# Kernel optimization log

Hardware: AMD Instinct MI355X
Metric: run time of the kernel (lower is better)

Reference implementation:

```python
import jax, jax.numpy as jnp
import numpy as np

B, L, D_MODEL, H = 2, 2048, 1024, 16
HD = D_MODEL // H  # head dim = 64


def setup_inputs() -> dict:
    key = jax.random.key(0)
    ks = jax.random.split(key, 11)
    s = 1.0 / np.sqrt(D_MODEL)
    inp = {
        "Q": jax.random.normal(ks[0], (B, L, D_MODEL), jnp.float32),
        "K": jax.random.normal(ks[1], (B, L, D_MODEL), jnp.float32),
        "V": jax.random.normal(ks[2], (B, L, D_MODEL), jnp.float32),
        "Wq": jax.random.normal(ks[3], (D_MODEL, D_MODEL), jnp.float32) * s,
        "bq": jnp.zeros((D_MODEL,), jnp.float32),
        "Wk": jax.random.normal(ks[4], (D_MODEL, D_MODEL), jnp.float32) * s,
        "bk": jnp.zeros((D_MODEL,), jnp.float32),
        "Wv": jax.random.normal(ks[5], (D_MODEL, D_MODEL), jnp.float32) * s,
        "bv": jnp.zeros((D_MODEL,), jnp.float32),
        "Wo": jax.random.normal(ks[6], (D_MODEL, D_MODEL), jnp.float32) * s,
        "bo": jnp.zeros((D_MODEL,), jnp.float32),
    }
    return inp


def _split_heads(x):
    # [B, L, H*D] -> [B, H, L, D]
    return x.reshape(B, L, H, HD).transpose(0, 2, 1, 3)


def reference(Q, K, V, Wq, bq, Wk, bk, Wv, bv, Wo, bo):
    q = _split_heads(Q @ Wq.T + bq)
    k = _split_heads(K @ Wk.T + bk)
    v = _split_heads(V @ Wv.T + bv)
    scale = 1.0 / jnp.sqrt(jnp.asarray(HD, q.dtype))
    # full [B, H, L, L] score matrix, as in the original bmm->softmax->bmm
    scores = jnp.einsum("bhqd,bhkd->bhqk", q, k) * scale
    attn = jax.nn.softmax(scores, axis=-1)
    o = jnp.einsum("bhqk,bhkd->bhqd", attn, v)
    o = o.transpose(0, 2, 1, 3).reshape(B, L, D_MODEL)  # concat heads
    return o @ Wo.T + bo
```

## Files before the change

### kernel.cpp

```cpp
#include <hip/hip_runtime.h>
#include <math.h>
#include <stdint.h>

typedef __bf16 bf16_t;
typedef __attribute__((ext_vector_type(2))) __bf16 bf16x2;
typedef __attribute__((ext_vector_type(8))) __bf16 bf16x8;
typedef __attribute__((ext_vector_type(4))) float f32x4;
typedef __attribute__((ext_vector_type(16))) float f32x16;
typedef __attribute__((address_space(1))) unsigned int gu32;
typedef __attribute__((address_space(3))) unsigned int lu32;

#define MFMA16(a, b, c) __builtin_amdgcn_mfma_f32_16x16x32_bf16((a), (b), (c), 0, 0, 0)
#define MFMA32(a, b, c) __builtin_amdgcn_mfma_f32_32x32x16_bf16((a), (b), (c), 0, 0, 0)

__device__ __forceinline__ void gll16(const void* g, void* l) {
    __builtin_amdgcn_global_load_lds((const gu32*)(uintptr_t)g,
                                     (lu32*)(uintptr_t)l, 16, 0, 0);
}

__device__ __forceinline__ bf16x8 ld_frag68(const bf16_t* p) {
    union { bf16x8 v; uint2 u[2]; } r;
    r.u[0] = *(const uint2*)p;
    r.u[1] = *(const uint2*)(p + 4);
    return r.v;
}

__global__ __launch_bounds__(256) void convert_all(
    const float* __restrict__ Q, const float* __restrict__ K, const float* __restrict__ V,
    const float* __restrict__ Wq, const float* __restrict__ Wk, const float* __restrict__ Wv,
    const float* __restrict__ Wo, bf16_t* __restrict__ dst) {
    size_t e0 = (size_t)blockIdx.x * 2048;
    const float* src; size_t off;
    if (e0 < 4194304)       { src = Q;  off = e0; }
    else if (e0 < 8388608)  { src = K;  off = e0 - 4194304; }
    else if (e0 < 12582912) { src = V;  off = e0 - 8388608; }
    else if (e0 < 13631488) { src = Wq; off = e0 - 12582912; }
    else if (e0 < 14680064) { src = Wk; off = e0 - 13631488; }
    else if (e0 < 15728640) { src = Wv; off = e0 - 14680064; }
    else                    { src = Wo; off = e0 - 15728640; }
#pragma unroll
    for (int p = 0; p < 2; ++p) {
        int t = p * 1024 + threadIdx.x * 4;
        float4 v = *(const float4*)(src + off + t);
        union { ushort4 u; bf16_t h[4]; } pk;
        pk.h[0] = (bf16_t)v.x; pk.h[1] = (bf16_t)v.y;
        pk.h[2] = (bf16_t)v.z; pk.h[3] = (bf16_t)v.w;
        *(ushort4*)(dst + e0 + t) = pk.u;
    }
}

__global__ __launch_bounds__(256) void qkv_gemm(
    const bf16_t* __restrict__ Qb, const bf16_t* __restrict__ Kb, const bf16_t* __restrict__ Vb,
    const bf16_t* __restrict__ Wqb, const bf16_t* __restrict__ Wkb, const bf16_t* __restrict__ Wvb,
    const float* __restrict__ bq, const float* __restrict__ bk, const float* __restrict__ bv,
    bf16_t* __restrict__ qo, bf16_t* __restrict__ ko, bf16_t* __restrict__ vT) {
    constexpr int Kdim = 1024, N = 1024;
    __shared__ __attribute__((aligned(16))) bf16_t smem[2 * 128 * 64];
    bf16_t* As = smem;
    bf16_t* Bs = smem + 128 * 64;

    const int tid = threadIdx.x, wave = tid >> 6, lane = tid & 63;
    const int z = blockIdx.z;
    const bf16_t* A = (z == 0) ? Qb : (z == 1) ? Kb : Vb;
    const bf16_t* W = (z == 0) ? Wqb : (z == 1) ? Wkb : Wvb;
    const float* bias = (z == 0) ? bq : (z == 1) ? bk : bv;
    const int bm = blockIdx.x * 128, bn = blockIdx.y * 128;
    const int l16 = lane & 15, quad = lane >> 4;
    const int wm = (wave >> 1) * 64, wn = (wave & 1) * 64;
    const int grow = lane >> 3, gcol = (lane & 7) * 8;

    f32x4 acc[4][4] = {};

    for (int k0 = 0; k0 < Kdim; k0 += 64) {
#pragma unroll
        for (int j = 0; j < 4; ++j) {
            int chunk = wave * 4 + j;
            int row = chunk * 8 + grow;
            gll16(A + (size_t)(bm + row) * Kdim + k0 + gcol, As + chunk * 512);
            gll16(W + (size_t)(bn + row) * Kdim + k0 + gcol, Bs + chunk * 512);
        }
        __syncthreads();
#pragma unroll
        for (int ks = 0; ks < 64; ks += 32) {
            bf16x8 af[4], bf[4];
#pragma unroll
            for (int i = 0; i < 4; ++i)
                af[i] = *(const bf16x8*)&As[(wm + i * 16 + l16) * 64 + ks + quad * 8];
#pragma unroll
            for (int i = 0; i < 4; ++i)
                bf[i] = *(const bf16x8*)&Bs[(wn + i * 16 + l16) * 64 + ks + quad * 8];
#pragma unroll
            for (int i = 0; i < 4; ++i)
#pragma unroll
                for (int j = 0; j < 4; ++j)
                    acc[i][j] = MFMA16(af[i], bf[j], acc[i][j]);
        }
        __syncthreads();
    }

    if (z < 2) {
        bf16_t* outp = (z == 0) ? qo : ko;
        const float sc = (z == 0) ? 0.18033688011112042f : 1.0f;
        constexpr int RST = 132;
#pragma unroll
        for (int p = 0; p < 2; ++p) {
            __syncthreads();
            if ((wave >> 1) == p) {
#pragma unroll
                for (int mi = 0; mi < 4; ++mi)
#pragma unroll
                    for (int nj = 0; nj < 4; ++nj) {
                        int col = wn + nj * 16 + l16;
                        float bv_ = bias[bn + col];
#pragma unroll
                        for (int r = 0; r < 4; ++r) {
                            int rp = mi * 16 + quad * 4 + r;
                            smem[rp * RST + col] = (bf16_t)((acc[mi][nj][r] + bv_) * sc);
                        }
                    }
            }
            __syncthreads();
            int rp = tid >> 2;
            int cb = (tid & 3) * 32;
            int row = bm + p * 64 + rp;
#pragma unroll
            for (int j = 0; j < 4; ++j) {
                uint2 lo = *(const uint2*)&smem[rp * RST + cb + j * 8];
                uint2 hi = *(const uint2*)&smem[rp * RST + cb + j * 8 + 4];
                *(uint4*)&outp[(size_t)row * N + bn + cb + j * 8] =
                    make_uint4(lo.x, lo.y, hi.x, hi.y);
            }
        }
    } else {
#pragma unroll
        for (int mi = 0; mi < 4; ++mi)
#pragma unroll
            for (int nj = 0; nj < 4; ++nj) {
                int col = bn + wn + nj * 16 + l16;
                int h = col >> 6, d = col & 63;
                float bv_ = bias[col];
                int row0 = bm + wm + mi * 16 + quad * 4;
                int bb = row0 >> 11, l = row0 & 2047;
                int lb = (l & ~12) | ((l & 4) << 1) | ((l & 8) >> 1);
                union { ushort4 u; bf16_t h4[4]; } pk;
#pragma unroll
                for (int r = 0; r < 4; ++r) pk.h4[r] = (bf16_t)(acc[mi][nj][r] + bv_);
                *(ushort4*)&vT[(((size_t)bb * 16 + h) * 64 + d) * 2048 + lb] = pk.u;
            }
    }
}

__global__ __launch_bounds__(256) void out_gemm(const bf16_t* __restrict__ A,
                                                const bf16_t* __restrict__ W,
                                                const float* __restrict__ bias,
                                                float* __restrict__ out) {
    constexpr int Kdim = 1024, N = 1024;
    __shared__ __attribute__((aligned(16))) bf16_t As[64 * 64];
    __shared__ __attribute__((aligned(16))) bf16_t Bs[128 * 64];
    const int tid = threadIdx.x, wave = tid >> 6, lane = tid & 63;
    const int bm = blockIdx.x * 64, bn = blockIdx.y * 128;
    const int l16 = lane & 15, quad = lane >> 4;
    const int wm = (wave >> 1) * 32, wn = (wave & 1) * 64;
    const int grow = lane >> 3, gcol = (lane & 7) * 8;
    f32x4 acc[2][4] = {};

    for (int k0 = 0; k0 < Kdim; k0 += 64) {
#pragma unroll
        for (int j = 0; j < 2; ++j) {
            int chunk = wave * 2 + j;
            int row = chunk * 8 + grow;
            gll16(A + (size_t)(bm + row) * Kdim + k0 + gcol, As + chunk * 512);
        }
#pragma unroll
        for (int j = 0; j < 4; ++j) {
            int chunk = wave * 4 + j;
            int row = chunk * 8 + grow;
            gll16(W + (size_t)(bn + row) * Kdim + k0 + gcol, Bs + chunk * 512);
        }
        __syncthreads();
#pragma unroll
        for (int ks = 0; ks < 64; ks += 32) {
            bf16x8 af[2], bf[4];
#pragma unroll
            for (int i = 0; i < 2; ++i)
                af[i] = *(const bf16x8*)&As[(wm + i * 16 + l16) * 64 + ks + quad * 8];
#pragma unroll
            for (int i = 0; i < 4; ++i)
                bf[i] = *(const bf16x8*)&Bs[(wn + i * 16 + l16) * 64 + ks + quad * 8];
#pragma unroll
            for (int i = 0; i < 2; ++i)
#pragma unroll
                for (int j = 0; j < 4; ++j)
                    acc[i][j] = MFMA16(af[i], bf[j], acc[i][j]);
        }
        __syncthreads();
    }
#pragma unroll
    for (int mi = 0; mi < 2; ++mi)
#pragma unroll
        for (int nj = 0; nj < 4; ++nj) {
            int col = bn + wn + nj * 16 + l16;
            float bv_ = bias[col];
#pragma unroll
            for (int r = 0; r < 4; ++r) {
                int row = bm + wm + mi * 16 + quad * 4 + r;
                out[(size_t)row * N + col] = acc[mi][nj][r] + bv_;
            }
        }
}

__global__ __launch_bounds__(256, 4) void attn6(const bf16_t* __restrict__ qo,
                                                const bf16_t* __restrict__ ko,
                                                const bf16_t* __restrict__ vT,
                                                bf16_t* __restrict__ Op,
                                                float* __restrict__ lpp) {
    constexpr int L = 2048, D = 1024, ST = 68;
    __shared__ __attribute__((aligned(16))) bf16_t smem[2 * 64 * ST];
    bf16_t* ksm = smem;
    bf16_t* vsm = smem + 64 * ST;

    const int tid = threadIdx.x, wave = tid >> 6, lane = tid & 63;
    const int l31 = lane & 31, hi = lane >> 5;
    const int b = blockIdx.x >> 4, h = blockIdx.x & 15;
    const int q0 = blockIdx.y * 128;
    const int split = blockIdx.z;
    bf16_t* Opart = Op + (size_t)split * 4194304;
    float* lpart = lpp + split * 65536;

    const int rloc = tid >> 2, cg = tid & 3;
    const bf16_t* kbase = ko + ((size_t)b * L + rloc) * D + h * 64 + cg * 16;
    const bf16_t* vbase = vT + (((size_t)b * 16 + h) * 64 + rloc) * L + cg * 16;

    bf16x8 qf[4];
    {
        const bf16_t* qptr = qo + ((size_t)b * L + q0 + wave * 32 + l31) * D + h * 64 + hi * 8;
#pragma unroll
        for (int ks = 0; ks < 4; ++ks) qf[ks] = *(const bf16x8*)(qptr + ks * 16);
    }

    f32x16 o0{}, o1{};
    float lpl = 0.f;

    const int kt0 = split * 16, kt1 = kt0 + 16;
    for (int kt = kt0; kt < kt1; ++kt) {
        const size_t koff = (size_t)(kt * 64) * D;
        const int voff = kt * 64;
        uint4 ka = *(const uint4*)(kbase + koff);
        uint4 kc = *(const uint4*)(kbase + koff + 8);
        uint4 va = *(const uint4*)(vbase + voff);
        uint4 vc = *(const uint4*)(vbase + voff + 8);
        __syncthreads();
        {
            bf16_t* kd = &ksm[rloc * ST + cg * 16];
            bf16_t* vd = &vsm[rloc * ST + cg * 16];
            *(uint2*)(kd + 0)  = make_uint2(ka.x, ka.y);
            *(uint2*)(kd + 4)  = make_uint2(ka.z, ka.w);
            *(uint2*)(kd + 8)  = make_uint2(kc.x, kc.y);
            *(uint2*)(kd + 12) = make_uint2(kc.z, kc.w);
            *(uint2*)(vd + 0)  = make_uint2(va.x, va.y);
            *(uint2*)(vd + 4)  = make_uint2(va.z, va.w);
            *(uint2*)(vd + 8)  = make_uint2(vc.x, vc.y);
            *(uint2*)(vd + 12) = make_uint2(vc.z, vc.w);
        }
        __syncthreads();

        f32x16 s0{}, s1{};
#pragma unroll
        for (int ks = 0; ks < 4; ++ks) {
            bf16x8 k0 = ld_frag68(&ksm[l31 * ST + ks * 16 + hi * 8]);
            bf16x8 k1 = ld_frag68(&ksm[(32 + l31) * ST + ks * 16 + hi * 8]);
            s0 = MFMA32(k0, qf[ks], s0);
            s1 = MFMA32(k1, qf[ks], s1);
        }

#pragma unroll
        for (int t = 0; t < 4; ++t) {
            union { bf16x8 v; bf16_t e[8]; } pf;
#pragma unroll
            for (int j = 0; j < 8; ++j) {
                float sv = (t < 2) ? s0[(t & 1) * 8 + j] : s1[(t & 1) * 8 + j];
                float p = __builtin_amdgcn_exp2f(sv);
                lpl += p;
                pf.e[j] = (bf16_t)p;
            }
            bf16x8 v0 = ld_frag68(&vsm[l31 * ST + t * 16 + hi * 8]);
            bf16x8 v1 = ld_frag68(&vsm[(32 + l31) * ST + t * 16 + hi * 8]);
            o0 = MFMA32(v0, pf.v, o0);
            o1 = MFMA32(v1, pf.v, o1);
        }
    }

    lpl += __shfl_xor(lpl, 32, 64);
    if (hi == 0)
        lpart[((size_t)b * 16 + h) * 2048 + q0 + wave * 32 + l31] = lpl;

    __syncthreads();
    bf16_t* ew = smem + wave * (32 * ST);
#pragma unroll
    for (int r = 0; r < 16; r += 2) {
        int d = (r & 3) + 8 * (r >> 2) + 4 * hi;
        *(bf16x2*)&ew[l31 * ST + d] = bf16x2{(bf16_t)o0[r], (bf16_t)o0[r + 1]};
        *(bf16x2*)&ew[l31 * ST + 32 + d] = bf16x2{(bf16_t)o1[r], (bf16_t)o1[r + 1]};
    }
#pragma unroll
    for (int p = 0; p < 4; ++p) {
        int rr = p * 8 + (lane >> 3);
        int cc = (lane & 7) * 8;
        uint2 lo = *(const uint2*)&ew[rr * ST + cc];
        uint2 hi2 = *(const uint2*)&ew[rr * ST + cc + 4];
        *(uint4*)&Opart[((size_t)b * L + q0 + wave * 32 + rr) * D + h * 64 + cc] =
            make_uint4(lo.x, lo.y, hi2.x, hi2.y);
    }
}

__global__ __launch_bounds__(256) void combine(const bf16_t* __restrict__ Op,
                                               const float* __restrict__ lpp,
                                               bf16_t* __restrict__ Ob) {
    const size_t c = (size_t)blockIdx.x * 256 + threadIdx.x;
    const int bl = (int)(c >> 7);
    const int h = ((int)c >> 3) & 15;
    const int bb = bl >> 11, l = bl & 2047;
    const int li = (bb * 16 + h) * 2048 + l;
    const float inv = 1.f / (lpp[li] + lpp[65536 + li]);
    union { uint4 u; bf16_t h8[8]; } a, b, o;
    a.u = *(const uint4*)(Op + c * 8);
    b.u = *(const uint4*)(Op + 4194304 + c * 8);
#pragma unroll
    for (int i = 0; i < 8; ++i)
        o.h8[i] = (bf16_t)(((float)a.h8[i] + (float)b.h8[i]) * inv);
    *(uint4*)(Ob + c * 8) = o.u;
}

extern "C" void kernel_launch(void* const* d_in, const int* in_sizes, int n_in,
                              void* d_out, int out_size, void* d_ws, size_t ws_size,
                              hipStream_t stream) {
    const float* Q  = (const float*)d_in[0];
    const float* Kx = (const float*)d_in[1];
    const float* V  = (const float*)d_in[2];
    const float* Wq = (const float*)d_in[3];
    const float* bq = (const float*)d_in[4];
    const float* Wk = (const float*)d_in[5];
    const float* bk = (const float*)d_in[6];
    const float* Wv = (const float*)d_in[7];
    const float* bv = (const float*)d_in[8];
    const float* Wo = (const float*)d_in[9];
    const float* bo = (const float*)d_in[10];

    bf16_t* ws0 = (bf16_t*)d_ws;
    bf16_t* Qb  = ws0;
    bf16_t* Kb  = ws0 + 4194304;
    bf16_t* Vb  = ws0 + 8388608;
    bf16_t* Wqb = ws0 + 12582912;
    bf16_t* Wkb = ws0 + 13631488;
    bf16_t* Wvb = ws0 + 14680064;
    bf16_t* Wob = ws0 + 15728640;
    bf16_t* vT  = ws0 + 16777216;
    bf16_t* Op  = Qb;
    bf16_t* Obf = Vb;
    float*  lpp = (float*)Wqb;
    bf16_t* qo = (bf16_t*)d_out;
    bf16_t* ko = qo + 4194304;

    convert_all<<<8192, 256, 0, stream>>>(Q, Kx, V, Wq, Wk, Wv, Wo, ws0);
    qkv_gemm<<<dim3(32, 8, 3), 256, 0, stream>>>(Qb, Kb, Vb, Wqb, Wkb, Wvb,
                                                 bq, bk, bv, qo, ko, vT);
    attn6<<<dim3(32, 16, 2), 256, 0, stream>>>(qo, ko, vT, Op, lpp);
    combine<<<2048, 256, 0, stream>>>(Op, lpp, Obf);
    out_gemm<<<dim3(64, 8), 256, 0, stream>>>(Obf, Wob, bo, (float*)d_out);
}
```

Measured before the change: 234.3 us.

## Double-buffer LDS tiles in QKV and output projection GEMMs

Both projection GEMMs now hold two LDS buffers. The global_load_lds for the next K tile is issued before the MFMA compute on the current tile, with one vmcnt wait and one barrier per iteration instead of two __syncthreads. This is meant to hide global-memory latency behind the matrix math. The cost is double the LDS footprint (64KB per block in qkv_gemm), which may reduce occupancy.

```diff
diff --git a/kernel.cpp b/kernel.cpp
--- a/kernel.cpp
+++ b/kernel.cpp
@@ -55,9 +55,7 @@
     const float* __restrict__ bq, const float* __restrict__ bk, const float* __restrict__ bv,
     bf16_t* __restrict__ qo, bf16_t* __restrict__ ko, bf16_t* __restrict__ vT) {
     constexpr int Kdim = 1024, N = 1024;
-    __shared__ __attribute__((aligned(16))) bf16_t smem[2 * 128 * 64];
-    bf16_t* As = smem;
-    bf16_t* Bs = smem + 128 * 64;
+    __shared__ __attribute__((aligned(16))) bf16_t smem[4 * 128 * 64];
 
     const int tid = threadIdx.x, wave = tid >> 6, lane = tid & 63;
     const int z = blockIdx.z;
@@ -71,7 +69,7 @@
 
     f32x4 acc[4][4] = {};
 
-    for (int k0 = 0; k0 < Kdim; k0 += 64) {
+    auto stage = [&](int k0, bf16_t* As, bf16_t* Bs) {
 #pragma unroll
         for (int j = 0; j < 4; ++j) {
             int chunk = wave * 4 + j;
@@ -79,7 +77,8 @@
             gll16(A + (size_t)(bm + row) * Kdim + k0 + gcol, As + chunk * 512);
             gll16(W + (size_t)(bn + row) * Kdim + k0 + gcol, Bs + chunk * 512);
         }
-        __syncthreads();
+    };
+    auto compute = [&](const bf16_t* As, const bf16_t* Bs) {
 #pragma unroll
         for (int ks = 0; ks < 64; ks += 32) {
             bf16x8 af[4], bf[4];
@@ -95,7 +94,24 @@
                 for (int j = 0; j < 4; ++j)
                     acc[i][j] = MFMA16(af[i], bf[j], acc[i][j]);
         }
-        __syncthreads();
+    };
+
+    stage(0, smem, smem + 8192);
+    asm volatile("s_waitcnt vmcnt(0)" ::: "memory");
+    __builtin_amdgcn_s_barrier();
+    int cur = 0;
+    for (int t = 0; t < 15; ++t) {
+        bf16_t* nb = smem + (cur ^ 1) * 16384;
+        stage((t + 1) * 64, nb, nb + 8192);
+        bf16_t* cb = smem + cur * 16384;
+        compute(cb, cb + 8192);
+        asm volatile("s_waitcnt vmcnt(0)" ::: "memory");
+        __builtin_amdgcn_s_barrier();
+        cur ^= 1;
+    }
+    {
+        bf16_t* cb = smem + cur * 16384;
+        compute(cb, cb + 8192);
     }
 
     if (z < 2) {
@@ -121,13 +137,13 @@
             }
             __syncthreads();
             int rp = tid >> 2;
-            int cb = (tid & 3) * 32;
+            int cb2 = (tid & 3) * 32;
             int row = bm + p * 64 + rp;
 #pragma unroll
             for (int j = 0; j < 4; ++j) {
-                uint2 lo = *(const uint2*)&smem[rp * RST + cb + j * 8];
-                uint2 hi = *(const uint2*)&smem[rp * RST + cb + j * 8 + 4];
-                *(uint4*)&outp[(size_t)row * N + bn + cb + j * 8] =
+                uint2 lo = *(const uint2*)&smem[rp * RST + cb2 + j * 8];
+                uint2 hi = *(const uint2*)&smem[rp * RST + cb2 + j * 8 + 4];
+                *(uint4*)&outp[(size_t)row * N + bn + cb2 + j * 8] =
                     make_uint4(lo.x, lo.y, hi.x, hi.y);
             }
         }
@@ -155,8 +171,7 @@
                                                 const float* __restrict__ bias,
                                                 float* __restrict__ out) {
     constexpr int Kdim = 1024, N = 1024;
-    __shared__ __attribute__((aligned(16))) bf16_t As[64 * 64];
-    __shared__ __attribute__((aligned(16))) bf16_t Bs[128 * 64];
+    __shared__ __attribute__((aligned(16))) bf16_t smem[2 * 12288];
     const int tid = threadIdx.x, wave = tid >> 6, lane = tid & 63;
     const int bm = blockIdx.x * 64, bn = blockIdx.y * 128;
     const int l16 = lane & 15, quad = lane >> 4;
@@ -164,7 +179,7 @@
     const int grow = lane >> 3, gcol = (lane & 7) * 8;
     f32x4 acc[2][4] = {};
 
-    for (int k0 = 0; k0 < Kdim; k0 += 64) {
+    auto stage = [&](int k0, bf16_t* As, bf16_t* Bs) {
 #pragma unroll
         for (int j = 0; j < 2; ++j) {
             int chunk = wave * 2 + j;
@@ -177,7 +192,8 @@
             int row = chunk * 8 + grow;
             gll16(W + (size_t)(bn + row) * Kdim + k0 + gcol, Bs + chunk * 512);
         }
-        __syncthreads();
+    };
+    auto compute = [&](const bf16_t* As, const bf16_t* Bs) {
 #pragma unroll
         for (int ks = 0; ks < 64; ks += 32) {
             bf16x8 af[2], bf[4];
@@ -193,8 +209,26 @@
                 for (int j = 0; j < 4; ++j)
                     acc[i][j] = MFMA16(af[i], bf[j], acc[i][j]);
         }
-        __syncthreads();
-    }
+    };
+
+    stage(0, smem, smem + 4096);
+    asm volatile("s_waitcnt vmcnt(0)" ::: "memory");
+    __builtin_amdgcn_s_barrier();
+    int cur = 0;
+    for (int t = 0; t < 15; ++t) {
+        bf16_t* nb = smem + (cur ^ 1) * 12288;
+        stage((t + 1) * 64, nb, nb + 4096);
+        bf16_t* cb = smem + cur * 12288;
+        compute(cb, cb + 4096);
+        asm volatile("s_waitcnt vmcnt(0)" ::: "memory");
+        __builtin_amdgcn_s_barrier();
+        cur ^= 1;
+    }
+    {
+        bf16_t* cb = smem + cur * 12288;
+        compute(cb, cb + 4096);
+    }
+
 #pragma unroll
     for (int mi = 0; mi < 2; ++mi)
 #pragma unroll
```

Measured after the change: 218.0 us. 6.9% less time.
